# Optimization experiments

Measured on AMD Instinct MI355X. Metric: run time of the kernel, lower is better.

## Reference

```python
import jax, jax.numpy as jnp
import numpy as np

CUTOFF = 3.0   # self.cutoff
RMIN = 3.5     # rmin in cutoff_function (note rmin > cutoff, faithful to source)
ETA = 4.0
N_RADIAL = 5
N_3BODY = 12
NATOMS = 2048
K = 48         # neighbors per atom (equal counts -> ragged loop becomes dense batch)
HID = 64
NPAIRS = NATOMS * K


def setup_inputs() -> dict:
    key = jax.random.key(0)
    ks = jax.random.split(key, 4)
    # displacements scaled so |rij| is mostly within a few Angstrom
    rij = jax.random.normal(ks[0], (NPAIRS, 3), jnp.float32) * 1.5
    # sorted-by-atom pair list with K neighbors per atom
    unique_i = jnp.repeat(jnp.arange(NATOMS, dtype=jnp.int64), K)
    W1 = jax.random.normal(ks[1], (N_RADIAL + N_3BODY, HID), jnp.float32) * 0.1
    b1 = jnp.zeros((HID,), jnp.float32)
    W2 = jax.random.normal(ks[2], (HID, HID), jnp.float32) * 0.1
    b2 = jnp.zeros((HID,), jnp.float32)
    W3 = jax.random.normal(ks[3], (HID, 1), jnp.float32) * 0.1
    b3 = jnp.zeros((1,), jnp.float32)
    return dict(rij=rij, unique_i=unique_i, W1=W1, b1=b1, W2=W2, b2=b2, W3=W3, b3=b3)


def _energy(rij, W1, b1, W2, b2, W3, b3):
    d = jnp.linalg.norm(rij, axis=1, keepdims=True)           # (P,1)
    diff_norm = rij / jnp.maximum(d, 1e-12)                   # F.normalize
    # pair cutoff (rmin=3.5, c=3.0 as in source)
    fc = jnp.where(d > RMIN,
                   0.5 + 0.5 * jnp.cos(jnp.pi * (d - RMIN) / (CUTOFF - RMIN)),
                   1.0)
    # radial Bessel basis, n = 1..5
    ns = jnp.arange(1, N_RADIAL + 1, dtype=rij.dtype)
    rbf = jnp.sqrt(2.0 / CUTOFF) * jnp.sin(ns * jnp.pi / CUTOFF * d) / d * fc  # (P,5)
    # 3-body Gaussian descriptors
    fcrik = (0.5 + 0.5 * jnp.cos(jnp.pi * d / CUTOFF))[:, 0]  # (P,)
    dn = diff_norm.reshape(NATOMS, K, 3)
    cosang = jnp.einsum('nkd,nld->nkl', dn, dn)               # (N,K,K) pairwise mm
    cosang = jnp.where(jnp.eye(K, dtype=bool)[None], 0.0, cosang)  # fill_diagonal_(0)
    mu = jnp.linspace(-1.0, 1.0, N_3BODY).astype(rij.dtype)
    w = fcrik.reshape(NATOMS, 1, K, 1)                        # fcrik broadcast on axis being summed
    g3b = jnp.sum(jnp.exp(-ETA * (cosang[..., None] - mu) ** 2) * w, axis=2)  # (N,K,12)
    g3b = g3b.reshape(NPAIRS, N_3BODY)
    desc = jnp.concatenate([rbf, g3b], axis=1)                # (P,17)
    h = jnp.tanh(desc @ W1 + b1)
    h = jnp.tanh(h @ W2 + b2)
    eij = h @ W3 + b3                                         # (P,1)
    return jnp.sum(eij * fc)


def reference(rij, unique_i, W1, b1, W2, b2, W3, b3):
    # Module output: gradients of total energy w.r.t. rij (written into beta)
    return jax.grad(_energy)(rij, W1, b1, W2, b2, W3, b3)
```

## Files before the change

### kernel.cpp

```cpp
#include <hip/hip_runtime.h>
#include <hip/hip_bf16.h>

#define NATOMS 2048
#define K 48
#define P (NATOMS * K)
#define NR 5
#define NM 12
#define ND 17
#define HID 64

#define PI_F 3.14159265358979f
#define CUT 3.0f
#define RMIN_F 3.5f
#define AFC (-6.28318530717959f)
#define POC (PI_F / CUT)
#define SQ 0.816496580927726f
#define E1C 1.45454545454545f
#define CMC (-0.132231404958678f)
#define N4L (-5.77078016355585f)
#define E1L (2.09846551402031f)
#define TL2 (2.88539008177793f)

__device__ unsigned short g_w1t[64 * 32];
__device__ unsigned short g_w2t[64 * 64];
__device__ unsigned short g_w2r[64 * 64];
__device__ unsigned short g_w1r[32 * 64];

using frag_ab = __attribute__((ext_vector_type(8))) short;
using frag_cd = __attribute__((ext_vector_type(4))) float;
using f2 = __attribute__((ext_vector_type(2))) float;
using f4 = __attribute__((ext_vector_type(4))) float;

__device__ __forceinline__ float fast_tanh(float x) {
    const float t = __builtin_amdgcn_exp2f(TL2 * x);
    return 1.0f - 2.0f * __builtin_amdgcn_rcpf(t + 1.0f);
}

__device__ __forceinline__ unsigned short f2bs(float x) {
    __hip_bfloat16 b = __float2bfloat16(x);
    return __builtin_bit_cast(unsigned short, b);
}

__device__ __forceinline__ float bs2f(unsigned short u) {
    return __builtin_bit_cast(float, ((unsigned)u) << 16);
}

template <int CTRL>
__device__ __forceinline__ float dpp_add(float x) {
    const int y = __builtin_amdgcn_update_dpp(
        0, __builtin_bit_cast(int, x), CTRL, 0xF, 0xF, true);
    return x + __builtin_bit_cast(float, y);
}

__global__ __launch_bounds__(256) void k_prep(const float* __restrict__ W1,
                                              const float* __restrict__ W2) {
    const int i = blockIdx.x * 256 + threadIdx.x;
    if (i < 2048) {
        const int n = i >> 5, k = i & 31;
        g_w1t[i] = (k < ND) ? f2bs(W1[k * HID + n]) : (unsigned short)0;
    } else if (i < 2048 + 4096) {
        const int j = i - 2048, n = j >> 6, k = j & 63;
        g_w2t[j] = f2bs(W2[k * HID + n]);
    } else if (i < 2048 + 8192) {
        const int j = i - (2048 + 4096);
        g_w2r[j] = f2bs(W2[j]);
    } else if (i < 2048 + 8192 + 2048) {
        const int j = i - (2048 + 8192), n = j >> 6;
        g_w1r[j] = (n < ND) ? f2bs(W1[j]) : (unsigned short)0;
    }
}

#define H1_OFF   0
#define ST_OFF   0
#define DESC_OFF 6912
#define GZ2_OFF  6912
#define SGD_OFF  6912
#define SGF_OFF  10560
#define SGU_OFF  11328
#define SS_OFF   13824
#define SE_OFF   18528
#define SU_OFF   19296
#define SFC_OFF  20064
#define SFK_OFF  20256
#define SM_BYTES 20448

__global__ __launch_bounds__(256, 6) void k_fused(const float* __restrict__ rij,
                                                  const float* __restrict__ b1,
                                                  const float* __restrict__ b2,
                                                  const float* __restrict__ W3,
                                                  const float* __restrict__ b3,
                                                  float* __restrict__ out) {
    __shared__ __align__(16) char smem[SM_BYTES];
    short*          h1S   = (short*)(smem + H1_OFF);
    unsigned short* sT    = (unsigned short*)(smem + ST_OFF);
    short*          descS = (short*)(smem + DESC_OFF);
    short*          gz2S  = (short*)(smem + GZ2_OFF);
    float*          sgd   = (float*)(smem + SGD_OFF);
    float*          sgf4  = (float*)(smem + SGF_OFF);
    float*          sgu4  = (float*)(smem + SGU_OFF);
    unsigned short* sS    = (unsigned short*)(smem + SS_OFF);
    float*          se    = (float*)(smem + SE_OFF);
    float*          su    = (float*)(smem + SU_OFF);
    float*          sfc   = (float*)(smem + SFC_OFF);
    float*          sfk   = (float*)(smem + SFK_OFF);

    const int t = threadIdx.x;
    const int base3 = blockIdx.x * (K * 3);
    const int w = t >> 6, lane = t & 63, quad = lane >> 4, lm = lane & 15;
    const int n0 = w * 16 + lm;

    const frag_ab wf1  = *(const frag_ab*)&g_w1t[n0 * 32 + quad * 8];
    const frag_ab wf2a = *(const frag_ab*)&g_w2t[n0 * 64 + quad * 8];
    const frag_ab wf2b = *(const frag_ab*)&g_w2t[n0 * 64 + 32 + quad * 8];
    const frag_ab wr2a = *(const frag_ab*)&g_w2r[n0 * 64 + quad * 8];
    const frag_ab wr2b = *(const frag_ab*)&g_w2r[n0 * 64 + 32 + quad * 8];
    const float bias1 = b1[n0];
    const float bias2 = b2[n0];
    const float w3n   = W3[n0];
    const float b3v   = b3[0];

    if (t < K) {
        const float x = rij[base3 + 3 * t];
        const float y = rij[base3 + 3 * t + 1];
        const float z = rij[base3 + 3 * t + 2];
        float s2 = fmaxf(x * x + y * y + z * z, 1e-24f);
        const float inv = __builtin_amdgcn_rsqf(s2);
        const float d = s2 * inv;
        *(f4*)&su[4 * t] = (f4){x * inv, y * inv, z * inv, d};
        sfk[t] = 0.5f + 0.5f * __cosf(POC * d);
        sfc[t] = (d > RMIN_F) ? (0.5f + 0.5f * __cosf(AFC * (d - RMIN_F))) : 1.0f;
#pragma unroll
        for (int c = ND; c < 32; c++) descS[t * 40 + c] = 0;
    }
    __syncthreads();

    if (t < 192) {
        const int k = t >> 2, ch = t & 3;
        const f4 uk = *(const f4*)&su[4 * k];
        const float* sul = &su[4 * (ch * 12)];
        f4 fkq[3];
        fkq[0] = *(const f4*)&sfk[ch * 12];
        fkq[1] = *(const f4*)&sfk[ch * 12 + 4];
        fkq[2] = *(const f4*)&sfk[ch * 12 + 8];
        f2 partv[6];
#pragma unroll
        for (int i = 0; i < 6; i++) partv[i] = (f2){0.0f, 0.0f};
#pragma unroll
        for (int li = 0; li < 12; li++) {
            const int l = ch * 12 + li;
            const f4 ul = *(const f4*)&sul[4 * li];
            float c = uk.x * ul.x + uk.y * ul.y + uk.z * ul.z;
            if (k == l) c = 0.0f;
            const float cp1 = c + 1.0f;
            const float e0 = __builtin_amdgcn_exp2f(N4L * cp1 * cp1) * fkq[li >> 2][li & 3];
            const float e1 = __builtin_amdgcn_exp2f(E1L * cp1);
            const float e2s = e1 * e1;
            const f2 e2v = {e2s, e2s};
            f2 tm = {e0, e0 * e1};
            partv[0] += tm;
#pragma unroll
            for (int i = 1; i < 6; i++) { tm *= e2v; partv[i] += tm; }
        }
#pragma unroll
        for (int i = 0; i < 6; i++) {
            partv[i].x = dpp_add<0x4E>(dpp_add<0xB1>(partv[i].x));
            partv[i].y = dpp_add<0x4E>(dpp_add<0xB1>(partv[i].y));
        }
        if (ch == 0) {
#pragma unroll
            for (int i = 0; i < 6; i++) {
                const int m0 = 2 * i, m1 = 2 * i + 1;
                descS[k * 40 + NR + m0] =
                    (short)f2bs(partv[i].x * __expf(CMC * (float)(m0 * m0)));
                descS[k * 40 + NR + m1] =
                    (short)f2bs(partv[i].y * __expf(CMC * (float)(m1 * m1)));
            }
        }
    } else {
#pragma unroll
        for (int r = 0; r < 4; r++) {
            const int idx = (t - 192) + 64 * r;
            if (idx < K * NR) {
                const int p = idx / NR, n = idx - NR * p;
                const float d = su[4 * p + 3];
                const float s = SQ * sfc[p] * __builtin_amdgcn_rcpf(d);
                descS[p * 40 + n] = (short)f2bs(s * __sinf((float)(n + 1) * POC * d));
            }
        }
    }
    __syncthreads();

    float t1[3][4];
    {
#pragma unroll
        for (int mt = 0; mt < 3; mt++) {
            const frag_ab a = *(const frag_ab*)&descS[(mt * 16 + lm) * 40 + quad * 8];
            frag_cd acc = {bias1, bias1, bias1, bias1};
            acc = __builtin_amdgcn_mfma_f32_16x16x32_bf16(a, wf1, acc, 0, 0, 0);
#pragma unroll
            for (int r = 0; r < 4; r++) {
                const float tv = fast_tanh(acc[r]);
                t1[mt][r] = tv;
                h1S[(mt * 16 + quad * 4 + r) * 72 + n0] = (short)f2bs(tv);
            }
        }
    }
    __syncthreads();

    {
#pragma unroll
        for (int mt = 0; mt < 3; mt++) {
            const frag_ab a0 = *(const frag_ab*)&h1S[(mt * 16 + lm) * 72 + quad * 8];
            const frag_ab a1 = *(const frag_ab*)&h1S[(mt * 16 + lm) * 72 + 32 + quad * 8];
            frag_cd acc = {bias2, bias2, bias2, bias2};
            acc = __builtin_amdgcn_mfma_f32_16x16x32_bf16(a0, wf2a, acc, 0, 0, 0);
            acc = __builtin_amdgcn_mfma_f32_16x16x32_bf16(a1, wf2b, acc, 0, 0, 0);
            const f4 fcv = *(const f4*)&sfc[mt * 16 + quad * 4];
            float ep[4];
#pragma unroll
            for (int r = 0; r < 4; r++) {
                const int row = mt * 16 + quad * 4 + r;
                const float tv = fast_tanh(acc[r]);
                ep[r] = tv * w3n;
                gz2S[row * 72 + n0] = (short)f2bs(fcv[r] * w3n * (1.0f - tv * tv));
            }
#pragma unroll
            for (int r = 0; r < 4; r++)
                ep[r] = dpp_add<0x118>(dpp_add<0x114>(dpp_add<0x112>(dpp_add<0x111>(ep[r]))));
            if (lm == 15) {
#pragma unroll
                for (int r = 0; r < 4; r++) se[w * 48 + mt * 16 + quad * 4 + r] = ep[r];
            }
        }
    }
    __syncthreads();

    {
#pragma unroll
        for (int mt = 0; mt < 3; mt++) {
            const frag_ab a0 = *(const frag_ab*)&gz2S[(mt * 16 + lm) * 72 + quad * 8];
            const frag_ab a1 = *(const frag_ab*)&gz2S[(mt * 16 + lm) * 72 + 32 + quad * 8];
            frag_cd acc = {0.0f, 0.0f, 0.0f, 0.0f};
            acc = __builtin_amdgcn_mfma_f32_16x16x32_bf16(a0, wr2a, acc, 0, 0, 0);
            acc = __builtin_amdgcn_mfma_f32_16x16x32_bf16(a1, wr2b, acc, 0, 0, 0);
#pragma unroll
            for (int r = 0; r < 4; r++) {
                const float g = acc[r] * (1.0f - t1[mt][r] * t1[mt][r]);
                h1S[(mt * 16 + quad * 4 + r) * 72 + n0] = (short)f2bs(g);
            }
        }
    }
    __syncthreads();

    for (int tid = w; tid < 6; tid += 4) {
        const int mt = tid >> 1, nt = tid & 1, n = nt * 16 + lm;
        const frag_ab b0 = *(const frag_ab*)&g_w1r[n * 64 + quad * 8];
        const frag_ab b1f = *(const frag_ab*)&g_w1r[n * 64 + 32 + quad * 8];
        const frag_ab a0 = *(const frag_ab*)&h1S[(mt * 16 + lm) * 72 + quad * 8];
        const frag_ab a1 = *(const frag_ab*)&h1S[(mt * 16 + lm) * 72 + 32 + quad * 8];
        frag_cd acc = {0.0f, 0.0f, 0.0f, 0.0f};
        acc = __builtin_amdgcn_mfma_f32_16x16x32_bf16(a0, b0, acc, 0, 0, 0);
        acc = __builtin_amdgcn_mfma_f32_16x16x32_bf16(a1, b1f, acc, 0, 0, 0);
        if (n < ND) {
            const int mm = n - NR;
            const float cmul = (n >= NR) ? __expf(CMC * (float)(mm * mm)) : 1.0f;
#pragma unroll
            for (int r = 0; r < 4; r++)
                sgd[(mt * 16 + quad * 4 + r) * 19 + n] = acc[r] * cmul;
        }
    }
    if (t < K)
        sgd[t * 19 + 17] = se[t] + se[48 + t] + se[96 + t] + se[144 + t] + b3v;
    __syncthreads();

    if (t < 192) {
        const int k = t >> 2, ch = t & 3;
        f2 gm[NM];
#pragma unroll
        for (int m = 0; m < NM; m++) {
            const float g = sgd[k * 19 + NR + m];
            gm[m] = (f2){g, (float)m * g};
        }
        const f4 uk = *(const f4*)&su[4 * k];
        const float* sul = &su[4 * (ch * 12)];
#pragma unroll
        for (int li = 0; li < 12; li++) {
            const int l = ch * 12 + li;
            const f4 ul = *(const f4*)&sul[4 * li];
            float c = uk.x * ul.x + uk.y * ul.y + uk.z * ul.z;
            if (k == l) c = 0.0f;
            const float cp1 = c + 1.0f;
            const float e0 = __builtin_amdgcn_exp2f(N4L * cp1 * cp1);
            const float x = __builtin_amdgcn_exp2f(E1L * cp1);
            const f2 xx = {x, x};
            f2 pd = gm[11];
#pragma unroll
            for (int m = 10; m >= 1; m--) pd = __builtin_elementwise_fma(pd, xx, gm[m]);
            const float Pv = fmaf(pd.x, x, gm[0].x);
            const float T = e0 * Pv;
            const float U = e0 * x * pd.y;
            const float Sp = fmaf(cp1, T, -(2.0f / 11.0f) * U);
            const float Sv = (k == l) ? 0.0f : (-8.0f) * Sp;
            sT[k * 49 + l] = f2bs(T);
            sS[k * 49 + l] = f2bs(Sv);
        }
    }
    __syncthreads();

    if (lane < K) {
        float s = 0.0f;
#pragma unroll
        for (int kk = 12 * w; kk < 12 * w + 12; kk++) s += bs2f(sT[kk * 49 + lane]);
        sgf4[w * 48 + lane] = s;

        const int k = lane;
        const float fk = sfk[k];
        float gx = 0.0f, gy = 0.0f, gz = 0.0f;
#pragma unroll
        for (int l = 12 * w; l < 12 * w + 12; l++) {
            const float wgt = fmaf(bs2f(sS[k * 49 + l]), sfk[l],
                                   bs2f(sS[l * 49 + k]) * fk);
            const f4 ul = *(const f4*)&su[4 * l];
            gx = fmaf(wgt, ul.x, gx);
            gy = fmaf(wgt, ul.y, gy);
            gz = fmaf(wgt, ul.z, gz);
        }
        sgu4[(w * 48 + k) * 3 + 0] = gx;
        sgu4[(w * 48 + k) * 3 + 1] = gy;
        sgu4[(w * 48 + k) * 3 + 2] = gz;
    }
    __syncthreads();

    if (t < K) {
        const float sgf_t = sgf4[t] + sgf4[48 + t] + sgf4[96 + t] + sgf4[144 + t];
        float gux = 0.0f, guy = 0.0f, guz = 0.0f;
#pragma unroll
        for (int ww = 0; ww < 4; ww++) {
            gux += sgu4[(ww * 48 + t) * 3 + 0];
            guy += sgu4[(ww * 48 + t) * 3 + 1];
            guz += sgu4[(ww * 48 + t) * 3 + 2];
        }
        const f4 uv = *(const f4*)&su[4 * t];
        const float d = uv.w;
        const float ux = uv.x, uy = uv.y, uz = uv.z;
        const float invd = __builtin_amdgcn_rcpf(d);
        float gfc = sgd[t * 19 + 17];
        float gdR = 0.0f;
#pragma unroll
        for (int n = 0; n < NR; n++) {
            const float bn = (float)(n + 1) * POC;
            float sn, cn;
            __sincosf(bn * d, &sn, &cn);
            const float g = sgd[t * 19 + n];
            gfc = fmaf(g, SQ * sn * invd, gfc);
            gdR = fmaf(g, SQ * (bn * cn - sn * invd) * invd, gdR);
        }
        const float fc = sfc[t];
        float dfc = 0.0f;
        if (d > RMIN_F) dfc = -0.5f * AFC * __sinf(AFC * (d - RMIN_F));
        const float dfcrik = -0.5f * POC * __sinf(POC * d);

        const float gd = fc * gdR + gfc * dfc + sgf_t * dfcrik;
        const float dot = gux * ux + guy * uy + guz * uz;

        out[base3 + 3 * t + 0] = fmaf(gd, ux, (gux - dot * ux) * invd);
        out[base3 + 3 * t + 1] = fmaf(gd, uy, (guy - dot * uy) * invd);
        out[base3 + 3 * t + 2] = fmaf(gd, uz, (guz - dot * uz) * invd);
    }
}

extern "C" void kernel_launch(void* const* d_in, const int* in_sizes, int n_in,
                              void* d_out, int out_size, void* d_ws, size_t ws_size,
                              hipStream_t stream) {
    (void)in_sizes; (void)n_in; (void)out_size; (void)d_ws; (void)ws_size;
    const float* rij = (const float*)d_in[0];
    const float* W1 = (const float*)d_in[2];
    const float* b1 = (const float*)d_in[3];
    const float* W2 = (const float*)d_in[4];
    const float* b2 = (const float*)d_in[5];
    const float* W3 = (const float*)d_in[6];
    const float* b3 = (const float*)d_in[7];
    float* out = (float*)d_out;

    k_prep<<<48, 256, 0, stream>>>(W1, W2);
    k_fused<<<NATOMS, 256, 0, stream>>>(rij, b1, b2, W3, b3, out);
}
```

Measured before the change: 93.52 us.

## Compute radial basis via sincos recurrence and disable unrolling to cut registers

The radial Bessel descriptor moves into the per-pair setup phase, where one sincos plus an angle-addition recurrence replaces five separate sin calls. The backward radial loop uses the same recurrence. The first-layer tanh values are no longer held across phases; they are re-read from shared bf16 storage. Many loops switch to unroll 1, which together with the dropped register arrays is meant to lower register pressure and raise occupancy, at the cost of loop overhead, lower ILP, and slightly lower precision from the bf16 tanh reload and the recurrence.

```diff
diff --git a/kernel.cpp b/kernel.cpp
--- a/kernel.cpp
+++ b/kernel.cpp
@@ -3,7 +3,6 @@
 
 #define NATOMS 2048
 #define K 48
-#define P (NATOMS * K)
 #define NR 5
 #define NM 12
 #define ND 17
@@ -15,7 +14,6 @@
 #define AFC (-6.28318530717959f)
 #define POC (PI_F / CUT)
 #define SQ 0.816496580927726f
-#define E1C 1.45454545454545f
 #define CMC (-0.132231404958678f)
 #define N4L (-5.77078016355585f)
 #define E1L (2.09846551402031f)
@@ -128,8 +126,20 @@
         const float d = s2 * inv;
         *(f4*)&su[4 * t] = (f4){x * inv, y * inv, z * inv, d};
         sfk[t] = 0.5f + 0.5f * __cosf(POC * d);
-        sfc[t] = (d > RMIN_F) ? (0.5f + 0.5f * __cosf(AFC * (d - RMIN_F))) : 1.0f;
-#pragma unroll
+        const float fc = (d > RMIN_F) ? (0.5f + 0.5f * __cosf(AFC * (d - RMIN_F))) : 1.0f;
+        sfc[t] = fc;
+        float s1, c1;
+        __sincosf(POC * d, &s1, &c1);
+        const float sc = SQ * fc * inv;
+        float sn = s1, cn = c1;
+#pragma unroll 1
+        for (int n = 0; n < NR; n++) {
+            descS[t * 40 + n] = (short)f2bs(sc * sn);
+            const float snx = sn * c1 + cn * s1;
+            cn = cn * c1 - sn * s1;
+            sn = snx;
+        }
+#pragma unroll 1
         for (int c = ND; c < 32; c++) descS[t * 40 + c] = 0;
     }
     __syncthreads();
@@ -138,21 +148,17 @@
         const int k = t >> 2, ch = t & 3;
         const f4 uk = *(const f4*)&su[4 * k];
         const float* sul = &su[4 * (ch * 12)];
-        f4 fkq[3];
-        fkq[0] = *(const f4*)&sfk[ch * 12];
-        fkq[1] = *(const f4*)&sfk[ch * 12 + 4];
-        fkq[2] = *(const f4*)&sfk[ch * 12 + 8];
         f2 partv[6];
 #pragma unroll
         for (int i = 0; i < 6; i++) partv[i] = (f2){0.0f, 0.0f};
-#pragma unroll
+#pragma unroll 1
         for (int li = 0; li < 12; li++) {
             const int l = ch * 12 + li;
             const f4 ul = *(const f4*)&sul[4 * li];
             float c = uk.x * ul.x + uk.y * ul.y + uk.z * ul.z;
             if (k == l) c = 0.0f;
             const float cp1 = c + 1.0f;
-            const float e0 = __builtin_amdgcn_exp2f(N4L * cp1 * cp1) * fkq[li >> 2][li & 3];
+            const float e0 = __builtin_amdgcn_exp2f(N4L * cp1 * cp1) * sfk[l];
             const float e1 = __builtin_amdgcn_exp2f(E1L * cp1);
             const float e2s = e1 * e1;
             const f2 e2v = {e2s, e2s};
@@ -176,82 +182,62 @@
                     (short)f2bs(partv[i].y * __expf(CMC * (float)(m1 * m1)));
             }
         }
-    } else {
+    }
+    __syncthreads();
+
+#pragma unroll 1
+    for (int mt = 0; mt < 3; mt++) {
+        const frag_ab a = *(const frag_ab*)&descS[(mt * 16 + lm) * 40 + quad * 8];
+        frag_cd acc = {bias1, bias1, bias1, bias1};
+        acc = __builtin_amdgcn_mfma_f32_16x16x32_bf16(a, wf1, acc, 0, 0, 0);
+#pragma unroll
+        for (int r = 0; r < 4; r++)
+            h1S[(mt * 16 + quad * 4 + r) * 72 + n0] = (short)f2bs(fast_tanh(acc[r]));
+    }
+    __syncthreads();
+
+#pragma unroll 1
+    for (int mt = 0; mt < 3; mt++) {
+        const frag_ab a0 = *(const frag_ab*)&h1S[(mt * 16 + lm) * 72 + quad * 8];
+        const frag_ab a1 = *(const frag_ab*)&h1S[(mt * 16 + lm) * 72 + 32 + quad * 8];
+        frag_cd acc = {bias2, bias2, bias2, bias2};
+        acc = __builtin_amdgcn_mfma_f32_16x16x32_bf16(a0, wf2a, acc, 0, 0, 0);
+        acc = __builtin_amdgcn_mfma_f32_16x16x32_bf16(a1, wf2b, acc, 0, 0, 0);
+        float ep[4];
 #pragma unroll
         for (int r = 0; r < 4; r++) {
-            const int idx = (t - 192) + 64 * r;
-            if (idx < K * NR) {
-                const int p = idx / NR, n = idx - NR * p;
-                const float d = su[4 * p + 3];
-                const float s = SQ * sfc[p] * __builtin_amdgcn_rcpf(d);
-                descS[p * 40 + n] = (short)f2bs(s * __sinf((float)(n + 1) * POC * d));
-            }
-        }
-    }
-    __syncthreads();
-
-    float t1[3][4];
-    {
-#pragma unroll
-        for (int mt = 0; mt < 3; mt++) {
-            const frag_ab a = *(const frag_ab*)&descS[(mt * 16 + lm) * 40 + quad * 8];
-            frag_cd acc = {bias1, bias1, bias1, bias1};
-            acc = __builtin_amdgcn_mfma_f32_16x16x32_bf16(a, wf1, acc, 0, 0, 0);
-#pragma unroll
-            for (int r = 0; r < 4; r++) {
-                const float tv = fast_tanh(acc[r]);
-                t1[mt][r] = tv;
-                h1S[(mt * 16 + quad * 4 + r) * 72 + n0] = (short)f2bs(tv);
-            }
-        }
-    }
-    __syncthreads();
-
-    {
-#pragma unroll
-        for (int mt = 0; mt < 3; mt++) {
-            const frag_ab a0 = *(const frag_ab*)&h1S[(mt * 16 + lm) * 72 + quad * 8];
-            const frag_ab a1 = *(const frag_ab*)&h1S[(mt * 16 + lm) * 72 + 32 + quad * 8];
-            frag_cd acc = {bias2, bias2, bias2, bias2};
-            acc = __builtin_amdgcn_mfma_f32_16x16x32_bf16(a0, wf2a, acc, 0, 0, 0);
-            acc = __builtin_amdgcn_mfma_f32_16x16x32_bf16(a1, wf2b, acc, 0, 0, 0);
-            const f4 fcv = *(const f4*)&sfc[mt * 16 + quad * 4];
-            float ep[4];
-#pragma unroll
-            for (int r = 0; r < 4; r++) {
-                const int row = mt * 16 + quad * 4 + r;
-                const float tv = fast_tanh(acc[r]);
-                ep[r] = tv * w3n;
-                gz2S[row * 72 + n0] = (short)f2bs(fcv[r] * w3n * (1.0f - tv * tv));
-            }
-#pragma unroll
-            for (int r = 0; r < 4; r++)
-                ep[r] = dpp_add<0x118>(dpp_add<0x114>(dpp_add<0x112>(dpp_add<0x111>(ep[r]))));
-            if (lm == 15) {
-#pragma unroll
-                for (int r = 0; r < 4; r++) se[w * 48 + mt * 16 + quad * 4 + r] = ep[r];
-            }
-        }
-    }
-    __syncthreads();
-
-    {
-#pragma unroll
-        for (int mt = 0; mt < 3; mt++) {
-            const frag_ab a0 = *(const frag_ab*)&gz2S[(mt * 16 + lm) * 72 + quad * 8];
-            const frag_ab a1 = *(const frag_ab*)&gz2S[(mt * 16 + lm) * 72 + 32 + quad * 8];
-            frag_cd acc = {0.0f, 0.0f, 0.0f, 0.0f};
-            acc = __builtin_amdgcn_mfma_f32_16x16x32_bf16(a0, wr2a, acc, 0, 0, 0);
-            acc = __builtin_amdgcn_mfma_f32_16x16x32_bf16(a1, wr2b, acc, 0, 0, 0);
-#pragma unroll
-            for (int r = 0; r < 4; r++) {
-                const float g = acc[r] * (1.0f - t1[mt][r] * t1[mt][r]);
-                h1S[(mt * 16 + quad * 4 + r) * 72 + n0] = (short)f2bs(g);
-            }
-        }
-    }
-    __syncthreads();
-
+            const int row = mt * 16 + quad * 4 + r;
+            const float tv = fast_tanh(acc[r]);
+            ep[r] = tv * w3n;
+            gz2S[row * 72 + n0] = (short)f2bs(sfc[row] * w3n * (1.0f - tv * tv));
+        }
+#pragma unroll
+        for (int r = 0; r < 4; r++)
+            ep[r] = dpp_add<0x118>(dpp_add<0x114>(dpp_add<0x112>(dpp_add<0x111>(ep[r]))));
+        if (lm == 15) {
+#pragma unroll
+            for (int r = 0; r < 4; r++) se[w * 48 + mt * 16 + quad * 4 + r] = ep[r];
+        }
+    }
+    __syncthreads();
+
+#pragma unroll 1
+    for (int mt = 0; mt < 3; mt++) {
+        const frag_ab a0 = *(const frag_ab*)&gz2S[(mt * 16 + lm) * 72 + quad * 8];
+        const frag_ab a1 = *(const frag_ab*)&gz2S[(mt * 16 + lm) * 72 + 32 + quad * 8];
+        frag_cd acc = {0.0f, 0.0f, 0.0f, 0.0f};
+        acc = __builtin_amdgcn_mfma_f32_16x16x32_bf16(a0, wr2a, acc, 0, 0, 0);
+        acc = __builtin_amdgcn_mfma_f32_16x16x32_bf16(a1, wr2b, acc, 0, 0, 0);
+#pragma unroll
+        for (int r = 0; r < 4; r++) {
+            const int row = mt * 16 + quad * 4 + r;
+            const float tv = bs2f((unsigned short)h1S[row * 72 + n0]);
+            h1S[row * 72 + n0] = (short)f2bs(acc[r] * (1.0f - tv * tv));
+        }
+    }
+    __syncthreads();
+
+#pragma unroll 1
     for (int tid = w; tid < 6; tid += 4) {
         const int mt = tid >> 1, nt = tid & 1, n = nt * 16 + lm;
         const frag_ab b0 = *(const frag_ab*)&g_w1r[n * 64 + quad * 8];
@@ -283,7 +269,7 @@
         }
         const f4 uk = *(const f4*)&su[4 * k];
         const float* sul = &su[4 * (ch * 12)];
-#pragma unroll
+#pragma unroll 1
         for (int li = 0; li < 12; li++) {
             const int l = ch * 12 + li;
             const f4 ul = *(const f4*)&sul[4 * li];
@@ -309,14 +295,14 @@
 
     if (lane < K) {
         float s = 0.0f;
-#pragma unroll
+#pragma unroll 1
         for (int kk = 12 * w; kk < 12 * w + 12; kk++) s += bs2f(sT[kk * 49 + lane]);
         sgf4[w * 48 + lane] = s;
 
         const int k = lane;
         const float fk = sfk[k];
         float gx = 0.0f, gy = 0.0f, gz = 0.0f;
-#pragma unroll
+#pragma unroll 1
         for (int l = 12 * w; l < 12 * w + 12; l++) {
             const float wgt = fmaf(bs2f(sS[k * 49 + l]), sfk[l],
                                    bs2f(sS[l * 49 + k]) * fk);
@@ -346,14 +332,18 @@
         const float invd = __builtin_amdgcn_rcpf(d);
         float gfc = sgd[t * 19 + 17];
         float gdR = 0.0f;
-#pragma unroll
+        float s1, c1;
+        __sincosf(POC * d, &s1, &c1);
+        float sn = s1, cn = c1, bn = POC;
+#pragma unroll 1
         for (int n = 0; n < NR; n++) {
-            const float bn = (float)(n + 1) * POC;
-            float sn, cn;
-            __sincosf(bn * d, &sn, &cn);
             const float g = sgd[t * 19 + n];
             gfc = fmaf(g, SQ * sn * invd, gfc);
             gdR = fmaf(g, SQ * (bn * cn - sn * invd) * invd, gdR);
+            const float snx = sn * c1 + cn * s1;
+            cn = cn * c1 - sn * s1;
+            sn = snx;
+            bn += POC;
         }
         const float fc = sfc[t];
         float dfc = 0.0f;
```

Result: no change. 93.49 us, median of 2 (-0.0%).
